# Optimization experiments

Measured on AMD Instinct MI355X. Metric: run time of the kernel, lower is better.

The kernel has to match this reference:

```python
import jax, jax.numpy as jnp
import numpy as np

B, T, D_IN, D_PROJ, D_OUT, MEM = 8, 2048, 1024, 1024, 1024, 40


def setup_inputs() -> dict:
    key = jax.random.key(0)
    k1, k2, k3, k4 = jax.random.split(key, 4)
    x = jax.random.normal(k1, (B, T, D_IN), dtype=jnp.float32)
    # xavier-uniform-style params
    lim1 = np.sqrt(6.0 / (D_IN + D_PROJ))
    lim2 = np.sqrt(6.0 / (D_PROJ + D_OUT))
    limm = np.sqrt(6.0 / (MEM + 1 + D_PROJ))
    W1 = jax.random.uniform(k2, (D_IN, D_PROJ), minval=-lim1, maxval=lim1, dtype=jnp.float32)
    W2 = jax.random.uniform(k3, (D_PROJ, D_OUT), minval=-lim2, maxval=lim2, dtype=jnp.float32)
    mw = jax.random.uniform(k4, (MEM + 1, D_PROJ), minval=-limm, maxval=limm, dtype=jnp.float32)
    mw = mw.at[0].set(0.0)  # row 0 zeroed at init (still trainable in the original)
    bias1 = jnp.ones((D_PROJ,), dtype=jnp.float32)
    bias2 = jnp.ones((D_OUT,), dtype=jnp.float32)
    return {"input_data": x, "W1": W1, "bias1": bias1, "W2": W2, "bias2": bias2,
            "memory_weights": mw}


def _fsmn_memory(p, memory_weights):
    # p: [B, T, D], memory_weights: [M+1, D]
    # Original gather index: mm[i,j] = i-j+1 for 0<=i-j<=M-1, else 0.
    # => out[b,i,d] = sum_{l=0}^{M-1} w[l+1,d]*p[b,i-l,d]
    #              + w[0,d] * (sum_j p[b,j,d] - sum_{l=0}^{M-1} p[b,i-l,d])
    M = memory_weights.shape[0] - 1
    b, t, d = p.shape
    # causal depthwise conv: taps w[1:] with lag l -> kernel position M-1-l
    rhs = memory_weights[1:][::-1].T[:, None, :]           # [D, 1, M]
    lhs = jnp.pad(p.transpose(0, 2, 1), ((0, 0), (0, 0), (M - 1, 0)))  # [B, D, T+M-1]
    band = jax.lax.conv_general_dilated(
        lhs, rhs, window_strides=(1,), padding='VALID',
        feature_group_count=d,
        dimension_numbers=('NCH', 'OIH', 'NCH')).transpose(0, 2, 1)    # [B, T, D]
    # in-band running sum via cumsum difference
    cs = jnp.cumsum(p, axis=1)                              # [B, T, D]
    band_sum = cs - jnp.pad(cs, ((0, 0), (M, 0), (0, 0)))[:, :t]
    total = cs[:, -1:]                                      # [B, 1, D]
    return band + memory_weights[0] * (total - band_sum)


def reference(input_data, W1, bias1, W2, bias2, memory_weights):
    p = jnp.matmul(input_data, W1) + bias1                  # [B, T, D_PROJ]
    p = _fsmn_memory(p, memory_weights)
    return jnp.matmul(p, W2) + bias2                        # [B, T, D_OUT]
```

## Files before the change

kernel.cpp:

```cpp
#include <hip/hip_runtime.h>

typedef __attribute__((ext_vector_type(8))) short bf16x8;
typedef __attribute__((ext_vector_type(4))) float f32x4;
typedef __attribute__((ext_vector_type(8))) unsigned short u16x8;

typedef const __attribute__((address_space(1))) void* as1cv;
typedef __attribute__((address_space(3))) void* as3v;

__device__ __forceinline__ unsigned short f2bf(float f) {
    union { float f; unsigned u; } x; x.f = f;
    unsigned r = x.u + 0x7FFFu + ((x.u >> 16) & 1u);
    return (unsigned short)(r >> 16);
}
__device__ __forceinline__ float bf2f(unsigned short u) {
    union { unsigned u; float f; } x; x.u = ((unsigned)u) << 16; return x.f;
}

__global__ void k_cvt_bf16(const float* __restrict__ in, unsigned short* __restrict__ out, long n) {
    long i = (long)blockIdx.x * blockDim.x + threadIdx.x;
    long stride = (long)gridDim.x * blockDim.x;
    long n4 = n >> 2;
    for (long j = i; j < n4; j += stride) {
        float4 v = ((const float4*)in)[j];
        ushort4 o;
        o.x = f2bf(v.x); o.y = f2bf(v.y); o.z = f2bf(v.z); o.w = f2bf(v.w);
        ((ushort4*)out)[j] = o;
    }
}

__global__ void k_transpose_bf16(const float* __restrict__ W1, unsigned short* __restrict__ W1t,
                                 const float* __restrict__ W2, unsigned short* __restrict__ W2t) {
    const int rows = 1024, cols = 1024;
    const float* W = blockIdx.z ? W2 : W1;
    unsigned short* Wt = blockIdx.z ? W2t : W1t;
    __shared__ float tile[64][65];
    int r0 = blockIdx.y * 64, c0 = blockIdx.x * 64;
    #pragma unroll
    for (int i = 0; i < 16; ++i) {
        int idx = threadIdx.x + i * 256;
        int r = idx >> 6, c = idx & 63;
        tile[r][c] = W[(long)(r0 + r) * cols + (c0 + c)];
    }
    __syncthreads();
    #pragma unroll
    for (int i = 0; i < 16; ++i) {
        int idx = threadIdx.x + i * 256;
        int r = idx >> 6, c = idx & 63;
        Wt[(long)(c0 + r) * rows + (r0 + c)] = f2bf(tile[c][r]);
    }
}

template<int OUT_BF16, int DO_COLSUM>
__global__ __launch_bounds__(512, 2) void k_gemm256(
    const unsigned short* __restrict__ A,
    const unsigned short* __restrict__ Bt,
    const float* __restrict__ bias,
    void* __restrict__ C,
    float* __restrict__ totals,
    int M, int N, int K)
{
    __shared__ unsigned short lds[2][4][8192];
    const int tid  = threadIdx.x;
    const int lane = tid & 63;
    const int w    = tid >> 6;
    const int wm   = w >> 2;
    const int wn   = w & 3;

    const int nwg = gridDim.x;
    const int cpx = nwg >> 3;
    const int wg  = (blockIdx.x & 7) * cpx + (blockIdx.x >> 3);
    const int nblks = N >> 8;
    const int mblk = wg / nblks, nblk = wg % nblks;
    const long m0 = (long)mblk << 8, n0 = (long)nblk << 8;

    const int segRow  = lane >> 3;
    const long segColE = (long)(((lane & 7) ^ segRow) << 3);

    const int rr = lane & 15, cc = lane >> 4;
    const int smask = (rr & 7) << 4;
    const int colSwz0 = (((cc * 16) ^ smask) >> 1);
    const int colSwz1 = (((64 + cc * 16) ^ smask) >> 1);

    auto stage = [&](int buf, int slot, const unsigned short* src, long rowBase, int kt) {
        #pragma unroll
        for (int g = 0; g < 2; ++g) {
            const int s = w + g * 8;
            const unsigned short* gp = src + (rowBase + s * 8 + segRow) * (long)K
                                           + (long)kt * 64 + segColE;
            __builtin_amdgcn_global_load_lds((as1cv)gp,
                (as3v)(&lds[buf][slot][s * 512 + lane * 8]), 16, 0, 0);
        }
    };

    f32x4 acc[8][4];
    #pragma unroll
    for (int i = 0; i < 8; ++i)
        #pragma unroll
        for (int j = 0; j < 4; ++j)
            acc[i][j] = (f32x4){0.f, 0.f, 0.f, 0.f};

    bf16x8 bfrag[4][2];
    const int bRowBase = (wn & 1) * 64;
    const int NK = K >> 6;
    const int ITERS = K >> 7;

#define VM4   asm volatile("s_waitcnt vmcnt(4)" ::: "memory")
#define PHASE(BUF, Q, STAGES, VMW) do {                                              \
    bf16x8 af0_0, af0_1, af1_0, af1_1;                                               \
    { const unsigned short* Ah = &lds[BUF][wm][0];                                   \
      af0_0 = *(const bf16x8*)(Ah + ((Q)*32 + rr) * 64 + colSwz0);                   \
      af0_1 = *(const bf16x8*)(Ah + ((Q)*32 + rr) * 64 + colSwz1);                   \
      af1_0 = *(const bf16x8*)(Ah + ((Q)*32 + 16 + rr) * 64 + colSwz0);              \
      af1_1 = *(const bf16x8*)(Ah + ((Q)*32 + 16 + rr) * 64 + colSwz1); }            \
    if ((Q) == 0) { const unsigned short* Bh = &lds[BUF][2 + (wn >> 1)][0];          \
      _Pragma("unroll")                                                              \
      for (int nj = 0; nj < 4; ++nj) {                                               \
        bfrag[nj][0] = *(const bf16x8*)(Bh + (bRowBase + nj*16 + rr) * 64 + colSwz0);\
        bfrag[nj][1] = *(const bf16x8*)(Bh + (bRowBase + nj*16 + rr) * 64 + colSwz1);\
      } }                                                                            \
    STAGES;                                                                          \
    VMW;                                                                             \
    __builtin_amdgcn_s_barrier();                                                    \
    asm volatile("s_waitcnt lgkmcnt(0)" ::: "memory");                               \
    __builtin_amdgcn_sched_barrier(0);                                               \
    __builtin_amdgcn_s_setprio(1);                                                   \
    _Pragma("unroll")                                                                \
    for (int nj = 0; nj < 4; ++nj) {                                                 \
      acc[2*(Q)][nj]   = __builtin_amdgcn_mfma_f32_16x16x32_bf16(af0_0, bfrag[nj][0], acc[2*(Q)][nj],   0,0,0); \
      acc[2*(Q)][nj]   = __builtin_amdgcn_mfma_f32_16x16x32_bf16(af0_1, bfrag[nj][1], acc[2*(Q)][nj],   0,0,0); \
      acc[2*(Q)+1][nj] = __builtin_amdgcn_mfma_f32_16x16x32_bf16(af1_0, bfrag[nj][0], acc[2*(Q)+1][nj], 0,0,0); \
      acc[2*(Q)+1][nj] = __builtin_amdgcn_mfma_f32_16x16x32_bf16(af1_1, bfrag[nj][1], acc[2*(Q)+1][nj], 0,0,0); \
    }                                                                                \
    __builtin_amdgcn_s_setprio(0);                                                   \
    __builtin_amdgcn_s_barrier();                                                    \
} while (0)

    stage(0, 0, A,  m0,       0);
    stage(0, 1, A,  m0 + 128, 0);
    stage(0, 2, Bt, n0,       0);
    stage(0, 3, Bt, n0 + 128, 0);
    stage(1, 2, Bt, n0,       1);
    stage(1, 3, Bt, n0 + 128, 1);
    VM4;
    __builtin_amdgcn_s_barrier();

    for (int it = 0; it < ITERS; ++it) {
        const int kt1 = 2 * it + 1;
        int kt2 = 2 * it + 2; if (kt2 >= NK) kt2 = 0;
        int kt3 = 2 * it + 3; if (kt3 >= NK) kt3 = 1;

        PHASE(0, 0, stage(1, 0, A,  m0,       kt1), );
        PHASE(0, 1, stage(1, 1, A,  m0 + 128, kt1), );
        PHASE(0, 2, { stage(0, 2, Bt, n0, kt2); stage(0, 3, Bt, n0 + 128, kt2); }, );
        PHASE(0, 3, , VM4);
        PHASE(1, 0, stage(0, 0, A,  m0,       kt2), );
        PHASE(1, 1, stage(0, 1, A,  m0 + 128, kt2), );
        PHASE(1, 2, { stage(1, 2, Bt, n0, kt3); stage(1, 3, Bt, n0 + 128, kt3); }, );
        PHASE(1, 3, , VM4);
    }
#undef PHASE
#undef VM4

    float cs[4] = {0.f, 0.f, 0.f, 0.f};
    #pragma unroll
    for (int mi = 0; mi < 8; ++mi) {
        const long rowb = m0 + wm * 128 + mi * 16 + cc * 4;
        #pragma unroll
        for (int nj = 0; nj < 4; ++nj) {
            const long col = n0 + wn * 64 + nj * 16 + rr;
            const float bv = bias[col];
            #pragma unroll
            for (int jj = 0; jj < 4; ++jj) {
                const float v = acc[mi][nj][jj] + bv;
                if (DO_COLSUM) cs[nj] += v;
                if (OUT_BF16) ((unsigned short*)C)[(rowb + jj) * N + col] = f2bf(v);
                else          ((float*)C)[(rowb + jj) * N + col] = v;
            }
        }
    }
    if (DO_COLSUM) {
        const int b = (int)(m0 >> 11);
        #pragma unroll
        for (int nj = 0; nj < 4; ++nj) {
            float c0 = cs[nj];
            c0 += __shfl_xor(c0, 16, 64);
            c0 += __shfl_xor(c0, 32, 64);
            if (cc == 0)
                atomicAdd(totals + b * 1024 + n0 + wn * 64 + nj * 16 + rr, c0);
        }
    }
}

#define FS_ROWS 167
__global__ __launch_bounds__(256, 2) void k_fsmn(
    const unsigned short* __restrict__ p,
    const float* __restrict__ mw,
    const float* __restrict__ total,
    unsigned short* __restrict__ p2,
    int T)
{
    __shared__ unsigned short sp[FS_ROWS][64];
    __shared__ float smw[41][64];
    const int b  = blockIdx.z;
    const int t0 = blockIdx.y * 128;
    const int d0 = blockIdx.x * 64;
    const int tid = threadIdx.x;

    for (int idx = tid; idx < 41 * 64; idx += 256) {
        int r = idx >> 6, c = idx & 63;
        smw[r][c] = mw[r * 1024 + d0 + c];
    }
    {
        const int row0 = tid >> 3;
        const int col8 = (tid & 7) * 8;
        #pragma unroll
        for (int i = 0; i < 6; ++i) {
            const int row = row0 + i * 32;
            if (row < FS_ROWS) {
                const int t = t0 + row - 39;
                u16x8 v = {0, 0, 0, 0, 0, 0, 0, 0};
                if (t >= 0)
                    v = *(const u16x8*)(p + ((long)b * T + t) * 1024 + d0 + col8);
                *(u16x8*)(&sp[row][col8]) = v;
            }
        }
    }
    __syncthreads();

    const int lane = tid & 63, wv = tid >> 6;
    const int d = d0 + lane;

    float m[40];
    #pragma unroll
    for (int l = 0; l < 40; ++l) m[l] = smw[l + 1][lane];
    const float m0v = smw[0][lane];
    const float tot = total[b * 1024 + d];

    #pragma unroll
    for (int pass = 0; pass < 2; ++pass) {
        const int obase = wv * 32 + pass * 16;
        float w[55];
        #pragma unroll
        for (int j = 0; j < 55; ++j) w[j] = bf2f(sp[obase + j][lane]);

        float acc[16];
        #pragma unroll
        for (int s = 0; s < 16; ++s) acc[s] = 0.f;
        #pragma unroll
        for (int lag = 0; lag < 40; ++lag) {
            const float mm = m[lag];
            #pragma unroll
            for (int s = 0; s < 16; ++s)
                acc[s] = fmaf(mm, w[s + 39 - lag], acc[s]);
        }

        float accw[16];
        {
            float S = 0.f;
            #pragma unroll
            for (int j = 0; j < 40; ++j) S += w[j];
            accw[0] = S;
            #pragma unroll
            for (int s = 1; s < 16; ++s) accw[s] = accw[s - 1] + w[s + 39] - w[s - 1];
        }

        unsigned short* ob = p2 + ((long)b * T + t0 + obase) * 1024 + d;
        #pragma unroll
        for (int s = 0; s < 16; ++s)
            ob[(long)s * 1024] = f2bf(acc[s] + m0v * (tot - accw[s]));
    }
}

extern "C" void kernel_launch(void* const* d_in, const int* in_sizes, int n_in,
                              void* d_out, int out_size, void* d_ws, size_t ws_size,
                              hipStream_t stream) {
    const float* x  = (const float*)d_in[0];
    const float* W1 = (const float*)d_in[1];
    const float* b1 = (const float*)d_in[2];
    const float* W2 = (const float*)d_in[3];
    const float* b2 = (const float*)d_in[4];
    const float* mw = (const float*)d_in[5];
    float* out = (float*)d_out;

    const int B = 8, T = 2048;
    const long M = (long)B * T;
    const int N = 1024, K = 1024;

    char* ws = (char*)d_ws;
    unsigned short* x_bf   = (unsigned short*)(ws);
    unsigned short* W1t    = (unsigned short*)(ws + 33554432L);
    unsigned short* W2t    = (unsigned short*)(ws + 35651584L);
    unsigned short* p_bf   = (unsigned short*)(ws + 37748736L);
    float*          totals = (float*)(ws + 71303168L);
    unsigned short* p2_bf  = x_bf;

    k_cvt_bf16<<<2048, 256, 0, stream>>>(x, x_bf, M * 1024);

    k_transpose_bf16<<<dim3(16, 16, 2), 256, 0, stream>>>(W1, W1t, W2, W2t);

    hipMemsetAsync(totals, 0, B * 1024 * sizeof(float), stream);

    k_gemm256<1, 1><<<dim3((int)((M / 256) * (N / 256))), 512, 0, stream>>>(
        x_bf, W1t, b1, (void*)p_bf, totals, (int)M, N, K);

    k_fsmn<<<dim3(1024 / 64, T / 128, B), 256, 0, stream>>>(p_bf, mw, totals, p2_bf, T);

    k_gemm256<0, 0><<<dim3((int)((M / 256) * (N / 256))), 512, 0, stream>>>(
        p2_bf, W2t, b2, (void*)out, nullptr, (int)M, N, K);
}
```

Before: 127.9 us.

## Fuse fp32-to-bf16 input conversion into first GEMM's A-tile loading

Drops the separate conversion kernel for x and has the first GEMM load fp32 A tiles into registers, convert them to bf16 and write them to swizzled LDS inside the pipeline. This removes one full pass writing and rereading a 32 MB bf16 copy of x plus a kernel launch. In exchange, each of the 16 column tiles re-reads and re-converts fp32 A (twice the bytes of bf16), uses more registers, and replaces async global-to-LDS loads with register-staged writes that may stall the MFMA pipeline.

```diff
diff --git a/kernel.cpp b/kernel.cpp
--- a/kernel.cpp
+++ b/kernel.cpp
@@ -14,18 +14,6 @@
 }
 __device__ __forceinline__ float bf2f(unsigned short u) {
     union { unsigned u; float f; } x; x.u = ((unsigned)u) << 16; return x.f;
-}
-
-__global__ void k_cvt_bf16(const float* __restrict__ in, unsigned short* __restrict__ out, long n) {
-    long i = (long)blockIdx.x * blockDim.x + threadIdx.x;
-    long stride = (long)gridDim.x * blockDim.x;
-    long n4 = n >> 2;
-    for (long j = i; j < n4; j += stride) {
-        float4 v = ((const float4*)in)[j];
-        ushort4 o;
-        o.x = f2bf(v.x); o.y = f2bf(v.y); o.z = f2bf(v.z); o.w = f2bf(v.w);
-        ((ushort4*)out)[j] = o;
-    }
 }
 
 __global__ void k_transpose_bf16(const float* __restrict__ W1, unsigned short* __restrict__ W1t,
@@ -50,9 +38,10 @@
     }
 }
 
-template<int OUT_BF16, int DO_COLSUM>
+template<int OUT_BF16, int DO_COLSUM, int A_FP32>
 __global__ __launch_bounds__(512, 2) void k_gemm256(
     const unsigned short* __restrict__ A,
+    const float* __restrict__ Af,
     const unsigned short* __restrict__ Bt,
     const float* __restrict__ bias,
     void* __restrict__ C,
@@ -75,6 +64,7 @@
 
     const int segRow  = lane >> 3;
     const long segColE = (long)(((lane & 7) ^ segRow) << 3);
+    const int colf = (lane & 7) * 8;
 
     const int rr = lane & 15, cc = lane >> 4;
     const int smask = (rr & 7) << 4;
@@ -89,6 +79,30 @@
                                            + (long)kt * 64 + segColE;
             __builtin_amdgcn_global_load_lds((as1cv)gp,
                 (as3v)(&lds[buf][slot][s * 512 + lane * 8]), 16, 0, 0);
+        }
+    };
+
+    float4 aR0[4], aR1[4];
+    auto aload = [&](float4* r, long rowBase, int kt) {
+        #pragma unroll
+        for (int g = 0; g < 2; ++g) {
+            const int s = w + g * 8;
+            const float* gp = Af + (rowBase + s * 8 + segRow) * (long)K
+                                 + (long)kt * 64 + colf;
+            r[2 * g]     = *(const float4*)(gp);
+            r[2 * g + 1] = *(const float4*)(gp + 4);
+        }
+    };
+    auto awrite = [&](int buf, int slot, float4* r) {
+        #pragma unroll
+        for (int g = 0; g < 2; ++g) {
+            const int s = w + g * 8;
+            uint4 pk;
+            pk.x = (unsigned)f2bf(r[2*g].x)   | ((unsigned)f2bf(r[2*g].y)   << 16);
+            pk.y = (unsigned)f2bf(r[2*g].z)   | ((unsigned)f2bf(r[2*g].w)   << 16);
+            pk.z = (unsigned)f2bf(r[2*g+1].x) | ((unsigned)f2bf(r[2*g+1].y) << 16);
+            pk.w = (unsigned)f2bf(r[2*g+1].z) | ((unsigned)f2bf(r[2*g+1].w) << 16);
+            *(uint4*)(&lds[buf][slot][s * 512 + segRow * 64 + (((lane & 7) ^ segRow) << 3)]) = pk;
         }
     };
 
@@ -135,28 +149,57 @@
     __builtin_amdgcn_s_barrier();                                                    \
 } while (0)
 
-    stage(0, 0, A,  m0,       0);
-    stage(0, 1, A,  m0 + 128, 0);
-    stage(0, 2, Bt, n0,       0);
-    stage(0, 3, Bt, n0 + 128, 0);
-    stage(1, 2, Bt, n0,       1);
-    stage(1, 3, Bt, n0 + 128, 1);
-    VM4;
-    __builtin_amdgcn_s_barrier();
-
-    for (int it = 0; it < ITERS; ++it) {
-        const int kt1 = 2 * it + 1;
-        int kt2 = 2 * it + 2; if (kt2 >= NK) kt2 = 0;
-        int kt3 = 2 * it + 3; if (kt3 >= NK) kt3 = 1;
-
-        PHASE(0, 0, stage(1, 0, A,  m0,       kt1), );
-        PHASE(0, 1, stage(1, 1, A,  m0 + 128, kt1), );
-        PHASE(0, 2, { stage(0, 2, Bt, n0, kt2); stage(0, 3, Bt, n0 + 128, kt2); }, );
-        PHASE(0, 3, , VM4);
-        PHASE(1, 0, stage(0, 0, A,  m0,       kt2), );
-        PHASE(1, 1, stage(0, 1, A,  m0 + 128, kt2), );
-        PHASE(1, 2, { stage(1, 2, Bt, n0, kt3); stage(1, 3, Bt, n0 + 128, kt3); }, );
-        PHASE(1, 3, , VM4);
+    if constexpr (A_FP32) {
+        aload(aR0, m0, 0);
+        aload(aR1, m0 + 128, 0);
+        stage(0, 2, Bt, n0,       0);
+        stage(0, 3, Bt, n0 + 128, 0);
+        stage(1, 2, Bt, n0,       1);
+        stage(1, 3, Bt, n0 + 128, 1);
+        asm volatile("s_waitcnt vmcnt(8)" ::: "memory");
+        awrite(0, 0, aR0);
+        awrite(0, 1, aR1);
+        asm volatile("s_waitcnt vmcnt(4) lgkmcnt(0)" ::: "memory");
+        __builtin_amdgcn_s_barrier();
+
+        for (int it = 0; it < ITERS; ++it) {
+            const int kt1 = 2 * it + 1;
+            int kt2 = 2 * it + 2; if (kt2 >= NK) kt2 = 0;
+            int kt3 = 2 * it + 3; if (kt3 >= NK) kt3 = 1;
+
+            PHASE(0, 0, aload(aR0, m0,       kt1), );
+            PHASE(0, 1, aload(aR1, m0 + 128, kt1), );
+            PHASE(0, 2, { stage(0, 2, Bt, n0, kt2); stage(0, 3, Bt, n0 + 128, kt2); }, );
+            PHASE(0, 3, { VM4; awrite(1, 0, aR0); awrite(1, 1, aR1); }, );
+            PHASE(1, 0, aload(aR0, m0,       kt2), );
+            PHASE(1, 1, aload(aR1, m0 + 128, kt2), );
+            PHASE(1, 2, { stage(1, 2, Bt, n0, kt3); stage(1, 3, Bt, n0 + 128, kt3); }, );
+            PHASE(1, 3, { VM4; awrite(0, 0, aR0); awrite(0, 1, aR1); }, );
+        }
+    } else {
+        stage(0, 0, A,  m0,       0);
+        stage(0, 1, A,  m0 + 128, 0);
+        stage(0, 2, Bt, n0,       0);
+        stage(0, 3, Bt, n0 + 128, 0);
+        stage(1, 2, Bt, n0,       1);
+        stage(1, 3, Bt, n0 + 128, 1);
+        VM4;
+        __builtin_amdgcn_s_barrier();
+
+        for (int it = 0; it < ITERS; ++it) {
+            const int kt1 = 2 * it + 1;
+            int kt2 = 2 * it + 2; if (kt2 >= NK) kt2 = 0;
+            int kt3 = 2 * it + 3; if (kt3 >= NK) kt3 = 1;
+
+            PHASE(0, 0, stage(1, 0, A,  m0,       kt1), );
+            PHASE(0, 1, stage(1, 1, A,  m0 + 128, kt1), );
+            PHASE(0, 2, { stage(0, 2, Bt, n0, kt2); stage(0, 3, Bt, n0 + 128, kt2); }, );
+            PHASE(0, 3, , VM4);
+            PHASE(1, 0, stage(0, 0, A,  m0,       kt2), );
+            PHASE(1, 1, stage(0, 1, A,  m0 + 128, kt2), );
+            PHASE(1, 2, { stage(1, 2, Bt, n0, kt3); stage(1, 3, Bt, n0 + 128, kt3); }, );
+            PHASE(1, 3, , VM4);
+        }
     }
 #undef PHASE
 #undef VM4
@@ -287,24 +330,21 @@
     const int N = 1024, K = 1024;
 
     char* ws = (char*)d_ws;
-    unsigned short* x_bf   = (unsigned short*)(ws);
+    unsigned short* p2_bf  = (unsigned short*)(ws);
     unsigned short* W1t    = (unsigned short*)(ws + 33554432L);
     unsigned short* W2t    = (unsigned short*)(ws + 35651584L);
     unsigned short* p_bf   = (unsigned short*)(ws + 37748736L);
     float*          totals = (float*)(ws + 71303168L);
-    unsigned short* p2_bf  = x_bf;
-
-    k_cvt_bf16<<<2048, 256, 0, stream>>>(x, x_bf, M * 1024);
 
     k_transpose_bf16<<<dim3(16, 16, 2), 256, 0, stream>>>(W1, W1t, W2, W2t);
 
     hipMemsetAsync(totals, 0, B * 1024 * sizeof(float), stream);
 
-    k_gemm256<1, 1><<<dim3((int)((M / 256) * (N / 256))), 512, 0, stream>>>(
-        x_bf, W1t, b1, (void*)p_bf, totals, (int)M, N, K);
+    k_gemm256<1, 1, 1><<<dim3((int)((M / 256) * (N / 256))), 512, 0, stream>>>(
+        nullptr, x, W1t, b1, (void*)p_bf, totals, (int)M, N, K);
 
     k_fsmn<<<dim3(1024 / 64, T / 128, B), 256, 0, stream>>>(p_bf, mw, totals, p2_bf, T);
 
-    k_gemm256<0, 0><<<dim3((int)((M / 256) * (N / 256))), 512, 0, stream>>>(
-        p2_bf, W2t, b2, (void*)out, nullptr, (int)M, N, K);
-}
+    k_gemm256<0, 0, 0><<<dim3((int)((M / 256) * (N / 256))), 512, 0, stream>>>(
+        p2_bf, nullptr, W2t, b2, (void*)out, nullptr, (int)M, N, K);
+}
```

After: 138.1 us. +8.0%, slower.
